# Optimization experiments

Measured on AMD Instinct MI355X. Metric: run time of the kernel, lower is better.

Reference implementation:

```python
import jax, jax.numpy as jnp
from jax import lax
import numpy as np

B, N, D_IN = 8, 8192, 16
GROUP_NUM, K = 512, 32
OUT_DIM, N_BLOCKS, DIM_EXP = 256, 2, 2
PREV_DIM = OUT_DIM // DIM_EXP   # 128
MID = OUT_DIM // 2              # bottleneck width in FeatureTransform
C_EXP = 2 * PREV_DIM + 3        # linear1 input channels
EPS = 1e-5                      # BatchNorm eps (eval mode, running stats mean=0 var=1)


def setup_inputs() -> dict:
    ks = jax.random.split(jax.random.key(0), 8)
    return {
        "xyz": jax.random.normal(ks[0], (B, N, 3), jnp.float32),
        "feat": jax.random.normal(ks[1], (B, N, D_IN), jnp.float32),
        "w_embed": jax.random.normal(ks[2], (PREV_DIM, D_IN), jnp.float32) * 0.1,
        "b_embed": jnp.zeros((PREV_DIM,), jnp.float32),
        "g_embed": jnp.ones((PREV_DIM,), jnp.float32),
        "be_embed": jnp.zeros((PREV_DIM,), jnp.float32),
        "w_lin1": jax.random.normal(ks[3], (OUT_DIM, C_EXP), jnp.float32) * 0.05,
        "g_lin1": jnp.ones((OUT_DIM,), jnp.float32),
        "be_lin1": jnp.zeros((OUT_DIM,), jnp.float32),
        "down_w": jax.random.normal(ks[4], (N_BLOCKS, MID, OUT_DIM), jnp.float32) * 0.05,
        "down_b": jnp.zeros((N_BLOCKS, MID), jnp.float32),
        "gd": jnp.ones((N_BLOCKS, MID), jnp.float32),
        "bd": jnp.zeros((N_BLOCKS, MID), jnp.float32),
        "up_w": jax.random.normal(ks[5], (N_BLOCKS, OUT_DIM, MID), jnp.float32) * 0.05,
        "up_b": jnp.zeros((N_BLOCKS, OUT_DIM), jnp.float32),
        "gu": jnp.ones((N_BLOCKS, OUT_DIM), jnp.float32),
        "bu": jnp.zeros((N_BLOCKS, OUT_DIM), jnp.float32),
    }


def _bn(x, g, b, axis):
    # eval-mode BatchNorm with running mean=0, var=1
    shp = [1] * x.ndim
    shp[axis] = -1
    return x / jnp.sqrt(1.0 + EPS) * g.reshape(shp) + b.reshape(shp)


def _fps(xyz, n):
    # deterministic FPS (eval mode): start from point farthest from origin
    Bb, Nn, _ = xyz.shape
    cur0 = jnp.argmax(jnp.sum(xyz * xyz, -1), axis=1)          # [B]
    mind0 = jnp.full((Bb, Nn), 1e10, xyz.dtype)

    def step(carry, _):
        cur, mind = carry
        c = jnp.take_along_axis(xyz, cur[:, None, None], axis=1)  # [B,1,3]
        mind = jnp.minimum(mind, jnp.sum((xyz - c) ** 2, -1))
        return (jnp.argmax(mind, axis=1), mind), cur

    _, sel = lax.scan(step, (cur0, mind0), None, length=n)     # sel: [n,B]
    return sel.T                                               # [B,n]


def _gather(points, idx):
    # points [B,N,C], idx [B,...] -> [B,...,C]
    Bb = points.shape[0]
    flat = idx.reshape(Bb, -1)
    out = jnp.take_along_axis(points, flat[:, :, None], axis=1)
    return out.reshape(idx.shape + (points.shape[-1],))


def _knn(k, ref, query):
    # squared dists, clamped at 0 as in pairwise_sq_dist
    d = (jnp.sum(query * query, -1)[:, :, None]
         + jnp.sum(ref * ref, -1)[:, None, :]
         - 2.0 * jnp.einsum('bsc,bnc->bsn', query, ref))
    d = jnp.maximum(d, 0.0)
    _, idx = lax.top_k(-d, k)
    return idx  # [B,S,k]


def reference(xyz, feat, w_embed, b_embed, g_embed, be_embed, w_lin1, g_lin1, be_lin1,
              down_w, down_b, gd, bd, up_w, up_b, gu, bu):
    # PointEmbed: conv1d(1x1) + BN + ReLU on per-point features -> [B,N,PREV_DIM]
    f0 = jnp.einsum('bnc,dc->bnd', feat, w_embed) + b_embed
    f0 = jax.nn.relu(_bn(f0, g_embed, be_embed, axis=2))

    # FpsKnnGroup
    sel = _fps(xyz, GROUP_NUM)                  # [B,G]
    lc_xyz = _gather(xyz, sel)                  # [B,G,3]
    lc_feat = _gather(f0, sel)                  # [B,G,PREV_DIM]
    nn_idx = _knn(K, xyz, lc_xyz)               # [B,G,K]
    knn_xyz = _gather(xyz, nn_idx)              # [B,G,K,3]
    knn_feat = jnp.concatenate([_gather(f0, nn_idx), knn_xyz], axis=-1)  # [B,G,K,PREV+3]

    # LocalGeoAgg, norm_type='mn40'
    anchor = lc_xyz[:, :, None, :]
    rel_raw = knn_xyz - anchor
    std = jnp.std(rel_raw, ddof=1) + 1e-5       # torch .std() is unbiased
    knn_xyz_n = rel_raw / std
    Bc = knn_feat.shape[0]
    expanded = jnp.concatenate(
        [knn_feat, jnp.broadcast_to(lc_feat[:, :, None, :], (Bc, GROUP_NUM, K, PREV_DIM))],
        axis=-1)                                # [B,G,K,C_EXP]
    x = jnp.einsum('bgkc,dc->bdgk', expanded, w_lin1)   # linear1 (no bias)
    x = jax.nn.relu(_bn(x, g_lin1, be_lin1, axis=1))    # [B,OUT_DIM,G,K]

    # GaussianPosEnc: rel = normalized knn_xyz (perm) minus raw lc_xyz center
    rel = knn_xyz_n.transpose(0, 3, 1, 2) - lc_xyz.transpose(0, 2, 1)[:, :, :, None]
    w = jnp.exp(-jnp.linalg.norm(rel, axis=1) / 2.0)    # sigma=1 -> 2*sigma^2=2
    x = x * w[:, None, :, :]

    # FeatureTransform residual bottlenecks
    for i in range(N_BLOCKS):
        h = jnp.einsum('bcgk,mc->bmgk', x, down_w[i]) + down_b[i][None, :, None, None]
        h = jax.nn.relu(_bn(h, gd[i], bd[i], axis=1))
        h = jnp.einsum('bcgk,mc->bmgk', h, up_w[i]) + up_b[i][None, :, None, None]
        h = _bn(h, gu[i], bu[i], axis=1)
        x = jax.nn.relu(h + x)

    # MaxMeanPool over K
    return jnp.max(x, axis=-1) + jnp.mean(x, axis=-1)   # [B,OUT_DIM,G]
```

## Files before the change

kernel.cpp:

```cpp
#include <hip/hip_runtime.h>

#define B_ 8
#define N_ 8192
#define DIN_ 16
#define G_ 512
#define K_ 32
#define OD_ 256
#define PD_ 128
#define MD_ 128
#define CE_ 259
#define EST 168
#define XST2 264
#define HST 136
#define AL1K 160

typedef __attribute__((ext_vector_type(8))) short short8t;
typedef __attribute__((ext_vector_type(4))) float f32x4;
#define MFMA16(a, b, c) __builtin_amdgcn_mfma_f32_16x16x32_bf16((a), (b), (c), 0, 0, 0)

__device__ __forceinline__ ushort bf16_rne(float x) {
    unsigned u = __float_as_uint(x);
    return (ushort)((u + 0x7FFFu + ((u >> 16) & 1u)) >> 16);
}
__device__ __forceinline__ void bf16_split(float x, ushort& h, ushort& l) {
    h = bf16_rne(x);
    float hf = __uint_as_float((unsigned)h << 16);
    l = bf16_rne(x - hf);
}

#define DPP_STEP_MAXF(x, ctrl) { int _t = __builtin_amdgcn_update_dpp(            \
        __float_as_int(x), __float_as_int(x), (ctrl), 0xF, 0xF, false);           \
        (x) = fmaxf((x), __int_as_float(_t)); }
#define DPP_STEP_MINF(x, ctrl) { int _t = __builtin_amdgcn_update_dpp(            \
        __float_as_int(x), __float_as_int(x), (ctrl), 0xF, 0xF, false);           \
        (x) = fminf((x), __int_as_float(_t)); }
#define DPP_STEP_MINU(x, ctrl) { int _t = __builtin_amdgcn_update_dpp(            \
        (int)(x), (int)(x), (ctrl), 0xF, 0xF, false);                             \
        unsigned _u = (unsigned)_t; (x) = ((x) < _u) ? (x) : _u; }

__device__ __forceinline__ float wave_max_f32(float x) {
    DPP_STEP_MAXF(x, 0x121); DPP_STEP_MAXF(x, 0x122);
    DPP_STEP_MAXF(x, 0x124); DPP_STEP_MAXF(x, 0x128);
    DPP_STEP_MAXF(x, 0x142); DPP_STEP_MAXF(x, 0x143);
    return __int_as_float(__builtin_amdgcn_readlane(__float_as_int(x), 63));
}
__device__ __forceinline__ float wave_min_f32(float x) {
    DPP_STEP_MINF(x, 0x121); DPP_STEP_MINF(x, 0x122);
    DPP_STEP_MINF(x, 0x124); DPP_STEP_MINF(x, 0x128);
    DPP_STEP_MINF(x, 0x142); DPP_STEP_MINF(x, 0x143);
    return __int_as_float(__builtin_amdgcn_readlane(__float_as_int(x), 63));
}
__device__ __forceinline__ unsigned wave_min_u32(unsigned x) {
    DPP_STEP_MINU(x, 0x121); DPP_STEP_MINU(x, 0x122);
    DPP_STEP_MINU(x, 0x124); DPP_STEP_MINU(x, 0x128);
    DPP_STEP_MINU(x, 0x142); DPP_STEP_MINU(x, 0x143);
    return (unsigned)__builtin_amdgcn_readlane((int)x, 63);
}

__global__ __launch_bounds__(256)
void prep_kernel(const float* __restrict__ w_lin1, const float* __restrict__ down_w,
                 const float* __restrict__ up_w, const float* __restrict__ w_embed,
                 float* __restrict__ wta, float* __restrict__ wEtg,
                 ushort* __restrict__ alf, ushort* __restrict__ adf,
                 ushort* __restrict__ auf) {
    int i = blockIdx.x * blockDim.x + threadIdx.x;
    if (i < PD_ * OD_) {
        int j = i >> 8, c = i & 255;
        wta[i] = w_lin1[c * CE_ + 131 + j];
    }
    if (i < DIN_ * PD_) {
        int r = i >> 7, c = i & 127;
        wEtg[i] = w_embed[c * DIN_ + r];
    }
    if (i < 5120) {
        int lane = i & 63, t = i >> 6;
        int kbi = t % 5, mtile = t / 5;
        int m = mtile * 16 + (lane & 15), g16 = lane >> 4;
        int dst = i * 8;
#pragma unroll
        for (int j = 0; j < 8; ++j) {
            int k = kbi * 32 + g16 * 8 + j;
            float v = (k < 131) ? w_lin1[m * CE_ + k] : 0.f;
            ushort h, l; bf16_split(v, h, l);
            alf[dst + j] = h; alf[dst + j + 40960] = l;
        }
    }
    if (i < 8192) {
        int lane = i & 63, t = i >> 6;
        int kbi = t & 7, mtile = (t >> 3) & 7, l = t >> 6;
        int m = mtile * 16 + (lane & 15), g16 = lane >> 4;
        int dst = i * 8;
#pragma unroll
        for (int j = 0; j < 8; ++j) {
            int k = kbi * 32 + g16 * 8 + j;
            float v = down_w[(l * MD_ + m) * OD_ + k];
            ushort h, lo; bf16_split(v, h, lo);
            adf[dst + j] = h; adf[dst + j + 65536] = lo;
        }
    }
    if (i < 8192) {
        int lane = i & 63, t = i >> 6;
        int kbi = t & 3, mtile = (t >> 2) & 15, l = t >> 6;
        int m = mtile * 16 + (lane & 15), g16 = lane >> 4;
        int dst = i * 8;
#pragma unroll
        for (int j = 0; j < 8; ++j) {
            int k = kbi * 32 + g16 * 8 + j;
            float v = up_w[(l * OD_ + m) * MD_ + k];
            ushort h, lo; bf16_split(v, h, lo);
            auf[dst + j] = h; auf[dst + j + 65536] = lo;
        }
    }
}

__global__ __launch_bounds__(512)
void fps_kernel(const float* __restrict__ xyz, int* __restrict__ sel) {
#pragma clang fp contract(off)
    __shared__ unsigned long long wred[2][8];
    __shared__ float4 wpt[2][8];
    __shared__ int sel_s[G_];
    int b = blockIdx.x, tid = threadIdx.x;
    const float* xb = xyz + (size_t)b * N_ * 3;
    float px[16], py[16], pz[16], mind[16];
    float bv = -1.f, bx = 0.f, by = 0.f, bz = 0.f; int bi = 0;
#pragma unroll
    for (int j = 0; j < 16; ++j) {
        int idx = tid + j * 512;
        px[j] = xb[idx * 3]; py[j] = xb[idx * 3 + 1]; pz[j] = xb[idx * 3 + 2];
        mind[j] = 1e10f;
        float ss = (px[j] * px[j] + py[j] * py[j]) + pz[j] * pz[j];
        if (ss > bv) { bv = ss; bi = idx; bx = px[j]; by = py[j]; bz = pz[j]; }
    }
    int wv = tid >> 6;
    {
        float wm = wave_max_f32(bv);
        unsigned mi = (bv == wm) ? (unsigned)bi : 0xFFFFFFFFu;
        unsigned wi = wave_min_u32(mi);
        if ((tid & 63) == 0)
            wred[0][wv] = ((unsigned long long)__float_as_uint(wm) << 32)
                        | (unsigned long long)(0xFFFFFFFFu - wi);
        if (bv == wm && (unsigned)bi == wi)
            wpt[0][wv] = make_float4(bx, by, bz, 0.f);
    }
    __syncthreads();
    unsigned long long best = wred[0][0]; int wb = 0;
#pragma unroll
    for (int i = 1; i < 8; ++i) { unsigned long long v = wred[0][i]; if (v > best) { best = v; wb = i; } }
    int cur = (int)(0xFFFFFFFFu - (unsigned)(best & 0xFFFFFFFFull));
    float4 cc = wpt[0][wb];
    float cx = cc.x, cy = cc.y, cz = cc.z;

    for (int it = 0; it < G_; ++it) {
        if (tid == 0) sel_s[it] = cur;
        bv = -1.f; bi = 0; bx = 0.f; by = 0.f; bz = 0.f;
#pragma unroll
        for (int j = 0; j < 16; ++j) {
            float dx = px[j] - cx, dy = py[j] - cy, dz = pz[j] - cz;
            float d = (dx * dx + dy * dy) + dz * dz;
            float m = fminf(mind[j], d); mind[j] = m;
            if (m > bv) { bv = m; bi = tid + j * 512; bx = px[j]; by = py[j]; bz = pz[j]; }
        }
        float wm = wave_max_f32(bv);
        unsigned mi = (bv == wm) ? (unsigned)bi : 0xFFFFFFFFu;
        unsigned wi = wave_min_u32(mi);
        int pb = (it + 1) & 1;
        if ((tid & 63) == 0)
            wred[pb][wv] = ((unsigned long long)__float_as_uint(wm) << 32)
                         | (unsigned long long)(0xFFFFFFFFu - wi);
        if (bv == wm && (unsigned)bi == wi)
            wpt[pb][wv] = make_float4(bx, by, bz, 0.f);
        __syncthreads();
        best = wred[pb][0]; wb = 0;
#pragma unroll
        for (int i = 1; i < 8; ++i) { unsigned long long v = wred[pb][i]; if (v > best) { best = v; wb = i; } }
        cur = (int)(0xFFFFFFFFu - (unsigned)(best & 0xFFFFFFFFull));
        cc = wpt[pb][wb];
        cx = cc.x; cy = cc.y; cz = cc.z;
    }
    __syncthreads();
    sel[b * G_ + tid] = sel_s[tid];
}

__global__ __launch_bounds__(256)
void knn_kernel(const float* __restrict__ xyz, const int* __restrict__ sel,
                int* __restrict__ nn) {
#pragma clang fp contract(off)
    __shared__ float dld[N_];
    __shared__ unsigned long long wred[2][4];
    __shared__ int nn_s[K_];
    int gb = blockIdx.x; int b = gb >> 9, s = gb & (G_ - 1);
    const float* xb = xyz + (size_t)b * N_ * 3;
    int q = sel[b * G_ + s];
    float qx = xb[q * 3], qy = xb[q * 3 + 1], qz = xb[q * 3 + 2];
    float qq = (qx * qx + qy * qy) + qz * qz;
    int tid = threadIdx.x;
    const float FINF = __builtin_inff();
    float lv = FINF; int li = tid;
#pragma unroll 4
    for (int j = 0; j < 32; ++j) {
        int n = tid + j * 256;
        float rx = xb[n * 3], ry = xb[n * 3 + 1], rz = xb[n * 3 + 2];
        float rr = (rx * rx + ry * ry) + rz * rz;
        float dt = (qx * rx + qy * ry) + qz * rz;
        float d = (qq + rr) - 2.0f * dt;
        d = fmaxf(d, 0.f);
        dld[n] = d;
        if (d < lv) { lv = d; li = n; }
    }
    {
        float wm = wave_min_f32(lv);
        unsigned mi = (lv == wm) ? (unsigned)li : 0xFFFFFFFFu;
        unsigned wi = wave_min_u32(mi);
        if ((tid & 63) == 0)
            wred[0][tid >> 6] = ((unsigned long long)__float_as_uint(wm) << 32)
                              | (unsigned long long)wi;
    }
    __syncthreads();
    unsigned long long best = wred[0][0];
#pragma unroll
    for (int i = 1; i < 4; ++i) { unsigned long long v = wred[0][i]; if (v < best) best = v; }
    int win = (int)(best & 0xFFFFFFFFull);

    for (int t = 0; t < K_; ++t) {
        if (tid == 0) nn_s[t] = win;
        if ((win & 255) == tid) {
            dld[win] = FINF;
            lv = FINF; li = tid;
            for (int j = 0; j < 32; ++j) {
                float d = dld[tid + j * 256];
                if (d < lv) { lv = d; li = tid + j * 256; }
            }
        }
        float wm = wave_min_f32(lv);
        unsigned mi = (lv == wm) ? (unsigned)li : 0xFFFFFFFFu;
        unsigned wi = wave_min_u32(mi);
        int pb = (t + 1) & 1;
        if ((tid & 63) == 0)
            wred[pb][tid >> 6] = ((unsigned long long)__float_as_uint(wm) << 32)
                               | (unsigned long long)wi;
        __syncthreads();
        best = wred[pb][0];
#pragma unroll
        for (int i = 1; i < 4; ++i) { unsigned long long v = wred[pb][i]; if (v < best) best = v; }
        win = (int)(best & 0xFFFFFFFFull);
    }
    if (tid < K_) nn[(size_t)gb * K_ + tid] = nn_s[tid];
}

__global__ void std_acc_kernel(const float* __restrict__ xyz, const int* __restrict__ sel,
                               const int* __restrict__ nn, double* __restrict__ acc) {
    int tot = B_ * G_ * K_;
    int stride = gridDim.x * blockDim.x;
    double ls = 0.0, lss = 0.0;
    for (int idx = blockIdx.x * blockDim.x + threadIdx.x; idx < tot; idx += stride) {
        int b = idx >> 14; int g = (idx >> 5) & (G_ - 1);
        int n = nn[idx]; int a = sel[b * G_ + g];
        const float* xb = xyz + (size_t)b * N_ * 3;
#pragma unroll
        for (int c = 0; c < 3; ++c) {
            float v = xb[n * 3 + c] - xb[a * 3 + c];
            ls += (double)v; lss += (double)v * (double)v;
        }
    }
#pragma unroll
    for (int off = 32; off > 0; off >>= 1) {
        ls += __shfl_down(ls, off); lss += __shfl_down(lss, off);
    }
    if ((threadIdx.x & 63) == 0) { atomicAdd(acc, ls); atomicAdd(acc + 1, lss); }
}

__global__ void std_fin_kernel(const double* __restrict__ acc, float* __restrict__ stdp) {
    double s = acc[0], ss = acc[1];
    double M = (double)(B_ * G_ * K_ * 3);
    double var = (ss - s * s / M) / (M - 1.0);
    stdp[0] = (float)sqrt(var) + 1e-5f;
}

__global__ __launch_bounds__(256, 3)
void group_kernel(const float* __restrict__ xyz, const float* __restrict__ feat,
                  const float* __restrict__ wEtg, const float* __restrict__ bE,
                  const float* __restrict__ gE, const float* __restrict__ beE,
                  const int* __restrict__ sel, const int* __restrict__ nn,
                  const float* __restrict__ wta,
                  const ushort* __restrict__ alf, const ushort* __restrict__ adf,
                  const ushort* __restrict__ auf,
                  const float* __restrict__ g_lin1, const float* __restrict__ be_lin1,
                  const float* __restrict__ down_b, const float* __restrict__ gd,
                  const float* __restrict__ bd,
                  const float* __restrict__ up_b, const float* __restrict__ gu,
                  const float* __restrict__ bu,
                  const float* __restrict__ stdp, float* __restrict__ out) {
    __shared__ __align__(16) ushort smem[25600];
    __shared__ float lcv_s[OD_];
    __shared__ float wk_s[K_];
    __shared__ int nns_s[K_];
    __shared__ float anch[3];
    ushort* XTh = smem;
    ushort* XTl = smem + 8448;
    ushort* HTh = smem + 16896;
    ushort* HTl = smem + 21248;
    ushort* Ehi = XTh;
    ushort* Elo = XTl;
    float* wEt = (float*)(smem + 16896);
    float* fL  = wEt + 2048;
    float* lcf = fL + 544;

    int gb = blockIdx.x; int b = gb >> 9, g = gb & (G_ - 1);
    int tid = threadIdx.x;
    const float* xb = xyz + (size_t)b * N_ * 3;
    int a = sel[b * G_ + g];
    if (tid < K_) nns_s[tid] = nn[(size_t)gb * K_ + tid];
    if (tid < 3)  anch[tid] = xb[a * 3 + tid];
    __syncthreads();

    for (int idx = tid; idx < DIN_ * PD_; idx += 256) wEt[idx] = wEtg[idx];
    const float* fb = feat + (size_t)b * N_ * DIN_;
    for (int idx = tid; idx < 33 * DIN_; idx += 256) {
        int k = idx >> 4, j = idx & 15;
        int n = (k < K_) ? nns_s[k] : a;
        fL[idx] = fb[(size_t)n * DIN_ + j];
    }
    __syncthreads();

    const float s_bn = 1.0f / sqrtf(1.0f + 1e-5f);
    for (int t = tid; t < 33 * 32; t += 256) {
        int k = t >> 5, c0 = (t & 31) * 4;
        const float* f = &fL[k * DIN_];
        float a0 = 0.f, a1 = 0.f, a2 = 0.f, a3 = 0.f;
#pragma unroll
        for (int i = 0; i < DIN_; ++i) {
            float4 w4 = *(const float4*)&wEt[i * PD_ + c0];
            float fv = f[i];
            a0 += w4.x * fv; a1 += w4.y * fv; a2 += w4.z * fv; a3 += w4.w * fv;
        }
        float4 b4  = *(const float4*)&bE[c0];
        float4 g4  = *(const float4*)&gE[c0];
        float4 be4 = *(const float4*)&beE[c0];
        float o0 = fmaxf((a0 + b4.x) * s_bn * g4.x + be4.x, 0.f);
        float o1 = fmaxf((a1 + b4.y) * s_bn * g4.y + be4.y, 0.f);
        float o2 = fmaxf((a2 + b4.z) * s_bn * g4.z + be4.z, 0.f);
        float o3 = fmaxf((a3 + b4.w) * s_bn * g4.w + be4.w, 0.f);
        if (k < K_) {
            ushort h0, l0, h1, l1, h2, l2, h3, l3;
            bf16_split(o0, h0, l0); bf16_split(o1, h1, l1);
            bf16_split(o2, h2, l2); bf16_split(o3, h3, l3);
            *(ushort4*)&Ehi[k * EST + c0] = make_ushort4(h0, h1, h2, h3);
            *(ushort4*)&Elo[k * EST + c0] = make_ushort4(l0, l1, l2, l3);
        } else {
            *(float4*)&lcf[c0] = make_float4(o0, o1, o2, o3);
        }
    }
    for (int idx = tid; idx < K_ * 32; idx += 256) {
        int k = idx >> 5, c = 128 + (idx & 31);
        ushort h = 0, l = 0;
        if (c < 131) { float v = xb[nns_s[k] * 3 + (c - 128)]; bf16_split(v, h, l); }
        Ehi[k * EST + c] = h; Elo[k * EST + c] = l;
    }
    if (tid < K_) {
#pragma clang fp contract(off)
        float sd = stdp[0];
        int n = nns_s[tid];
        float rx = (xb[n * 3]     - anch[0]) / sd - anch[0];
        float ry = (xb[n * 3 + 1] - anch[1]) / sd - anch[1];
        float rz = (xb[n * 3 + 2] - anch[2]) / sd - anch[2];
        float nrm = sqrtf((rx * rx + ry * ry) + rz * rz);
        wk_s[tid] = expf(-0.5f * nrm);
    }
    __syncthreads();
    {
        float s = 0.f;
        for (int j = 0; j < PD_; ++j) s += wta[j * OD_ + tid] * lcf[j];
        lcv_s[tid] = s;
    }
    __syncthreads();

    int wv = tid >> 6, lane = tid & 63;
    int g16 = lane >> 4, r16 = lane & 15;
    int lane8 = lane * 8;

    f32x4 accl[4][2];
#pragma unroll
    for (int mt = 0; mt < 4; ++mt) {
        int mc = 64 * wv + 16 * mt + 4 * g16;
        float4 lv = *(const float4*)&lcv_s[mc];
        f32x4 iv = {lv.x, lv.y, lv.z, lv.w};
        accl[mt][0] = iv; accl[mt][1] = iv;
    }
    {
        int eb0 = r16 * EST + g16 * 8;
        int eb1 = (r16 + 16) * EST + g16 * 8;
        for (int kbi = 0; kbi < 5; ++kbi) {
            int kb = kbi * 32;
            short8t eh0 = *(const short8t*)&Ehi[eb0 + kb];
            short8t el0 = *(const short8t*)&Elo[eb0 + kb];
            short8t eh1 = *(const short8t*)&Ehi[eb1 + kb];
            short8t el1 = *(const short8t*)&Elo[eb1 + kb];
#pragma unroll
            for (int mt = 0; mt < 4; ++mt) {
                const ushort* wp = alf + (((4 * wv + mt) * 5 + kbi) << 9) + lane8;
                short8t wh = *(const short8t*)wp;
                short8t wl = *(const short8t*)(wp + 40960);
                accl[mt][0] = MFMA16(wh, eh0, accl[mt][0]);
                accl[mt][1] = MFMA16(wh, eh1, accl[mt][1]);
                accl[mt][0] = MFMA16(wh, el0, accl[mt][0]);
                accl[mt][1] = MFMA16(wh, el1, accl[mt][1]);
                accl[mt][0] = MFMA16(wl, eh0, accl[mt][0]);
                accl[mt][1] = MFMA16(wl, eh1, accl[mt][1]);
            }
        }
    }
    __syncthreads();
    {
        float w0 = wk_s[r16], w1 = wk_s[r16 + 16];
#pragma unroll
        for (int mt = 0; mt < 4; ++mt) {
            int mc = 64 * wv + 16 * mt + 4 * g16;
            float4 gg = *(const float4*)&g_lin1[mc];
            float4 bb = *(const float4*)&be_lin1[mc];
            float ga[4] = {gg.x, gg.y, gg.z, gg.w};
            float ba[4] = {bb.x, bb.y, bb.z, bb.w};
            ushort h0[4], l0[4], h1[4], l1[4];
#pragma unroll
            for (int r = 0; r < 4; ++r) {
                float v0 = fmaxf(accl[mt][0][r] * s_bn * ga[r] + ba[r], 0.f) * w0;
                float v1 = fmaxf(accl[mt][1][r] * s_bn * ga[r] + ba[r], 0.f) * w1;
                bf16_split(v0, h0[r], l0[r]);
                bf16_split(v1, h1[r], l1[r]);
            }
            *(ushort4*)&XTh[r16 * XST2 + mc] = make_ushort4(h0[0], h0[1], h0[2], h0[3]);
            *(ushort4*)&XTl[r16 * XST2 + mc] = make_ushort4(l0[0], l0[1], l0[2], l0[3]);
            *(ushort4*)&XTh[(r16 + 16) * XST2 + mc] = make_ushort4(h1[0], h1[1], h1[2], h1[3]);
            *(ushort4*)&XTl[(r16 + 16) * XST2 + mc] = make_ushort4(l1[0], l1[1], l1[2], l1[3]);
        }
    }
    __syncthreads();

    int xbo0 = r16 * XST2 + g16 * 8;
    int xbo1 = (r16 + 16) * XST2 + g16 * 8;
    int hbo0 = r16 * HST + g16 * 8;
    int hbo1 = (r16 + 16) * HST + g16 * 8;
    const f32x4 zz = {0.f, 0.f, 0.f, 0.f};
    const float inv_k = 1.0f / 32.0f;

    for (int l = 0; l < 2; ++l) {
        f32x4 accd[2][2];
        accd[0][0] = zz; accd[0][1] = zz; accd[1][0] = zz; accd[1][1] = zz;
        for (int kbi = 0; kbi < 8; ++kbi) {
            int kb = kbi * 32;
            short8t xh0 = *(const short8t*)&XTh[xbo0 + kb];
            short8t xl0 = *(const short8t*)&XTl[xbo0 + kb];
            short8t xh1 = *(const short8t*)&XTh[xbo1 + kb];
            short8t xl1 = *(const short8t*)&XTl[xbo1 + kb];
#pragma unroll
            for (int mt = 0; mt < 2; ++mt) {
                const ushort* wp = adf + (((l * 8 + (2 * wv + mt)) * 8 + kbi) << 9) + lane8;
                short8t wh = *(const short8t*)wp;
                short8t wl = *(const short8t*)(wp + 65536);
                accd[mt][0] = MFMA16(wh, xh0, accd[mt][0]);
                accd[mt][1] = MFMA16(wh, xh1, accd[mt][1]);
                accd[mt][0] = MFMA16(wh, xl0, accd[mt][0]);
                accd[mt][1] = MFMA16(wh, xl1, accd[mt][1]);
                accd[mt][0] = MFMA16(wl, xh0, accd[mt][0]);
                accd[mt][1] = MFMA16(wl, xh1, accd[mt][1]);
            }
        }
#pragma unroll
        for (int mt = 0; mt < 2; ++mt) {
            int mc = 32 * wv + 16 * mt + 4 * g16;
            float4 db = *(const float4*)&down_b[l * MD_ + mc];
            float4 gv = *(const float4*)&gd[l * MD_ + mc];
            float4 bv = *(const float4*)&bd[l * MD_ + mc];
            float dba[4] = {db.x, db.y, db.z, db.w};
            float gva[4] = {gv.x, gv.y, gv.z, gv.w};
            float bva[4] = {bv.x, bv.y, bv.z, bv.w};
            ushort h0[4], l0[4], h1[4], l1[4];
#pragma unroll
            for (int r = 0; r < 4; ++r) {
                float v0 = fmaxf((accd[mt][0][r] + dba[r]) * s_bn * gva[r] + bva[r], 0.f);
                float v1 = fmaxf((accd[mt][1][r] + dba[r]) * s_bn * gva[r] + bva[r], 0.f);
                bf16_split(v0, h0[r], l0[r]);
                bf16_split(v1, h1[r], l1[r]);
            }
            *(ushort4*)&HTh[r16 * HST + mc] = make_ushort4(h0[0], h0[1], h0[2], h0[3]);
            *(ushort4*)&HTl[r16 * HST + mc] = make_ushort4(l0[0], l0[1], l0[2], l0[3]);
            *(ushort4*)&HTh[(r16 + 16) * HST + mc] = make_ushort4(h1[0], h1[1], h1[2], h1[3]);
            *(ushort4*)&HTl[(r16 + 16) * HST + mc] = make_ushort4(l1[0], l1[1], l1[2], l1[3]);
        }
        __syncthreads();

        f32x4 accu[4][2];
#pragma unroll
        for (int mt = 0; mt < 4; ++mt) { accu[mt][0] = zz; accu[mt][1] = zz; }
        for (int kbi = 0; kbi < 4; ++kbi) {
            int kb = kbi * 32;
            short8t hh0 = *(const short8t*)&HTh[hbo0 + kb];
            short8t hl0 = *(const short8t*)&HTl[hbo0 + kb];
            short8t hh1 = *(const short8t*)&HTh[hbo1 + kb];
            short8t hl1 = *(const short8t*)&HTl[hbo1 + kb];
#pragma unroll
            for (int mt = 0; mt < 4; ++mt) {
                const ushort* wp = auf + (((l * 16 + (4 * wv + mt)) * 4 + kbi) << 9) + lane8;
                short8t wh = *(const short8t*)wp;
                short8t wl = *(const short8t*)(wp + 65536);
                accu[mt][0] = MFMA16(wh, hh0, accu[mt][0]);
                accu[mt][1] = MFMA16(wh, hh1, accu[mt][1]);
                accu[mt][0] = MFMA16(wh, hl0, accu[mt][0]);
                accu[mt][1] = MFMA16(wh, hl1, accu[mt][1]);
                accu[mt][0] = MFMA16(wl, hh0, accu[mt][0]);
                accu[mt][1] = MFMA16(wl, hh1, accu[mt][1]);
            }
        }
#pragma unroll
        for (int mt = 0; mt < 4; ++mt) {
            int mc = 64 * wv + 16 * mt + 4 * g16;
            float4 ub = *(const float4*)&up_b[l * OD_ + mc];
            float4 gv = *(const float4*)&gu[l * OD_ + mc];
            float4 bv = *(const float4*)&bu[l * OD_ + mc];
            float uba[4] = {ub.x, ub.y, ub.z, ub.w};
            float gva[4] = {gv.x, gv.y, gv.z, gv.w};
            float bva[4] = {bv.x, bv.y, bv.z, bv.w};
            ushort4 xh0 = *(const ushort4*)&XTh[r16 * XST2 + mc];
            ushort4 xl0 = *(const ushort4*)&XTl[r16 * XST2 + mc];
            ushort4 xh1 = *(const ushort4*)&XTh[(r16 + 16) * XST2 + mc];
            ushort4 xl1 = *(const ushort4*)&XTl[(r16 + 16) * XST2 + mc];
            ushort xha0[4] = {xh0.x, xh0.y, xh0.z, xh0.w};
            ushort xla0[4] = {xl0.x, xl0.y, xl0.z, xl0.w};
            ushort xha1[4] = {xh1.x, xh1.y, xh1.z, xh1.w};
            ushort xla1[4] = {xl1.x, xl1.y, xl1.z, xl1.w};
            float nx0[4], nx1[4];
#pragma unroll
            for (int r = 0; r < 4; ++r) {
                float xf0 = __uint_as_float((unsigned)xha0[r] << 16) + __uint_as_float((unsigned)xla0[r] << 16);
                float xf1 = __uint_as_float((unsigned)xha1[r] << 16) + __uint_as_float((unsigned)xla1[r] << 16);
                float v0 = (accu[mt][0][r] + uba[r]) * s_bn * gva[r] + bva[r];
                float v1 = (accu[mt][1][r] + uba[r]) * s_bn * gva[r] + bva[r];
                nx0[r] = fmaxf(v0 + xf0, 0.f);
                nx1[r] = fmaxf(v1 + xf1, 0.f);
            }
            if (l == 0) {
                ushort h0[4], l0[4], h1[4], l1[4];
#pragma unroll
                for (int r = 0; r < 4; ++r) {
                    bf16_split(nx0[r], h0[r], l0[r]);
                    bf16_split(nx1[r], h1[r], l1[r]);
                }
                *(ushort4*)&XTh[r16 * XST2 + mc] = make_ushort4(h0[0], h0[1], h0[2], h0[3]);
                *(ushort4*)&XTl[r16 * XST2 + mc] = make_ushort4(l0[0], l0[1], l0[2], l0[3]);
                *(ushort4*)&XTh[(r16 + 16) * XST2 + mc] = make_ushort4(h1[0], h1[1], h1[2], h1[3]);
                *(ushort4*)&XTl[(r16 + 16) * XST2 + mc] = make_ushort4(l1[0], l1[1], l1[2], l1[3]);
            } else {
#pragma unroll
                for (int r = 0; r < 4; ++r) {
                    float mx = fmaxf(nx0[r], nx1[r]);
                    float sm = nx0[r] + nx1[r];
#pragma unroll
                    for (int off = 1; off < 16; off <<= 1) {
                        mx = fmaxf(mx, __shfl_xor(mx, off));
                        sm += __shfl_xor(sm, off);
                    }
                    if (r16 == 0)
                        out[((size_t)(b * OD_ + mc + r)) * G_ + g] = mx + sm * inv_k;
                }
            }
        }
        __syncthreads();
    }
}

extern "C" void kernel_launch(void* const* d_in, const int* in_sizes, int n_in,
                              void* d_out, int out_size, void* d_ws, size_t ws_size,
                              hipStream_t stream) {
    const float* xyz     = (const float*)d_in[0];
    const float* feat    = (const float*)d_in[1];
    const float* w_embed = (const float*)d_in[2];
    const float* b_embed = (const float*)d_in[3];
    const float* g_embed = (const float*)d_in[4];
    const float* be_embed= (const float*)d_in[5];
    const float* w_lin1  = (const float*)d_in[6];
    const float* g_lin1  = (const float*)d_in[7];
    const float* be_lin1 = (const float*)d_in[8];
    const float* down_w  = (const float*)d_in[9];
    const float* down_b  = (const float*)d_in[10];
    const float* gd      = (const float*)d_in[11];
    const float* bd      = (const float*)d_in[12];
    const float* up_w    = (const float*)d_in[13];
    const float* up_b    = (const float*)d_in[14];
    const float* gu      = (const float*)d_in[15];
    const float* bu      = (const float*)d_in[16];
    float* out = (float*)d_out;

    char* w = (char*)d_ws;
    float* wta   = (float*)w;  w += PD_ * OD_ * 4;
    float* wEtg  = (float*)w;  w += DIN_ * PD_ * 4;
    ushort* alf  = (ushort*)w; w += 2 * 40960 * 2;
    ushort* adf  = (ushort*)w; w += 2 * 65536 * 2;
    ushort* auf  = (ushort*)w; w += 2 * 65536 * 2;
    int* sel     = (int*)w;    w += B_ * G_ * 4;
    int* nn      = (int*)w;    w += B_ * G_ * K_ * 4;
    double* acc  = (double*)w; w += 16;
    float* stdp  = (float*)w;

    hipMemsetAsync(acc, 0, 2 * sizeof(double), stream);
    prep_kernel<<<256, 256, 0, stream>>>(w_lin1, down_w, up_w, w_embed,
                                         wta, wEtg, alf, adf, auf);
    fps_kernel<<<B_, 512, 0, stream>>>(xyz, sel);
    knn_kernel<<<B_ * G_, 256, 0, stream>>>(xyz, sel, nn);
    std_acc_kernel<<<256, 256, 0, stream>>>(xyz, sel, nn, acc);
    std_fin_kernel<<<1, 1, 0, stream>>>(acc, stdp);
    group_kernel<<<B_ * G_, 256, 0, stream>>>(xyz, feat, wEtg, b_embed, g_embed, be_embed,
        sel, nn, wta, alf, adf, auf, g_lin1, be_lin1, down_b, gd, bd, up_b, gu, bu, stdp, out);
}
```

Before: 1.102 ms.

## Stage FPS points in LDS, pack distance math into float2, drop winner-coordinate broadcast

The FPS kernel now copies the batch's xyz into shared memory as separate x/y/z arrays. Each thread keeps its 16 points as packed float2 vectors so the distance and min-update can use packed FP32 ops. Instead of the winning thread writing its coordinates to shared memory, every thread reads the new centroid from the shared copy by index. This simplifies the per-iteration argmax and cuts register moves in the serial 512-iteration loop, at the cost of 96KB of LDS and an extra shared read per iteration.

```diff
diff --git a/kernel.cpp b/kernel.cpp
--- a/kernel.cpp
+++ b/kernel.cpp
@@ -16,6 +16,7 @@
 
 typedef __attribute__((ext_vector_type(8))) short short8t;
 typedef __attribute__((ext_vector_type(4))) float f32x4;
+typedef __attribute__((ext_vector_type(2))) float v2f;
 #define MFMA16(a, b, c) __builtin_amdgcn_mfma_f32_16x16x32_bf16((a), (b), (c), 0, 0, 0)
 
 __device__ __forceinline__ ushort bf16_rne(float x) {
@@ -116,21 +117,30 @@
 __global__ __launch_bounds__(512)
 void fps_kernel(const float* __restrict__ xyz, int* __restrict__ sel) {
 #pragma clang fp contract(off)
+    __shared__ float sx[N_], sy[N_], sz[N_];
     __shared__ unsigned long long wred[2][8];
-    __shared__ float4 wpt[2][8];
     __shared__ int sel_s[G_];
     int b = blockIdx.x, tid = threadIdx.x;
     const float* xb = xyz + (size_t)b * N_ * 3;
-    float px[16], py[16], pz[16], mind[16];
-    float bv = -1.f, bx = 0.f, by = 0.f, bz = 0.f; int bi = 0;
-#pragma unroll
-    for (int j = 0; j < 16; ++j) {
-        int idx = tid + j * 512;
-        px[j] = xb[idx * 3]; py[j] = xb[idx * 3 + 1]; pz[j] = xb[idx * 3 + 2];
-        mind[j] = 1e10f;
-        float ss = (px[j] * px[j] + py[j] * py[j]) + pz[j] * pz[j];
-        if (ss > bv) { bv = ss; bi = idx; bx = px[j]; by = py[j]; bz = pz[j]; }
-    }
+    for (int i = tid; i < N_; i += 512) {
+        sx[i] = xb[i * 3]; sy[i] = xb[i * 3 + 1]; sz[i] = xb[i * 3 + 2];
+    }
+    __syncthreads();
+    v2f px2[8], py2[8], pz2[8], mind2[8];
+    float bv = -1.f; int bj = 0;
+#pragma unroll
+    for (int p = 0; p < 8; ++p) {
+        int i0 = tid + (2 * p) * 512, i1 = tid + (2 * p + 1) * 512;
+        px2[p] = (v2f){sx[i0], sx[i1]};
+        py2[p] = (v2f){sy[i0], sy[i1]};
+        pz2[p] = (v2f){sz[i0], sz[i1]};
+        mind2[p] = (v2f){1e10f, 1e10f};
+        v2f ss = px2[p] * px2[p] + py2[p] * py2[p];
+        ss = ss + pz2[p] * pz2[p];
+        if (ss[0] > bv) { bv = ss[0]; bj = 2 * p; }
+        if (ss[1] > bv) { bv = ss[1]; bj = 2 * p + 1; }
+    }
+    int bi = tid + bj * 512;
     int wv = tid >> 6;
     {
         float wm = wave_max_f32(bv);
@@ -139,27 +149,31 @@
         if ((tid & 63) == 0)
             wred[0][wv] = ((unsigned long long)__float_as_uint(wm) << 32)
                         | (unsigned long long)(0xFFFFFFFFu - wi);
-        if (bv == wm && (unsigned)bi == wi)
-            wpt[0][wv] = make_float4(bx, by, bz, 0.f);
-    }
-    __syncthreads();
-    unsigned long long best = wred[0][0]; int wb = 0;
-#pragma unroll
-    for (int i = 1; i < 8; ++i) { unsigned long long v = wred[0][i]; if (v > best) { best = v; wb = i; } }
+    }
+    __syncthreads();
+    unsigned long long best = wred[0][0];
+#pragma unroll
+    for (int i = 1; i < 8; ++i) { unsigned long long v = wred[0][i]; if (v > best) best = v; }
     int cur = (int)(0xFFFFFFFFu - (unsigned)(best & 0xFFFFFFFFull));
-    float4 cc = wpt[0][wb];
-    float cx = cc.x, cy = cc.y, cz = cc.z;
 
     for (int it = 0; it < G_; ++it) {
         if (tid == 0) sel_s[it] = cur;
-        bv = -1.f; bi = 0; bx = 0.f; by = 0.f; bz = 0.f;
+        float cx = sx[cur], cy = sy[cur], cz = sz[cur];
+        v2f cx2 = (v2f){cx, cx}, cy2 = (v2f){cy, cy}, cz2 = (v2f){cz, cz};
+#pragma unroll
+        for (int p = 0; p < 8; ++p) {
+            v2f dx = px2[p] - cx2, dy = py2[p] - cy2, dz = pz2[p] - cz2;
+            v2f d = dx * dx + dy * dy;
+            d = d + dz * dz;
+            mind2[p] = __builtin_elementwise_min(mind2[p], d);
+        }
+        bv = -1.f; bj = 0;
 #pragma unroll
         for (int j = 0; j < 16; ++j) {
-            float dx = px[j] - cx, dy = py[j] - cy, dz = pz[j] - cz;
-            float d = (dx * dx + dy * dy) + dz * dz;
-            float m = fminf(mind[j], d); mind[j] = m;
-            if (m > bv) { bv = m; bi = tid + j * 512; bx = px[j]; by = py[j]; bz = pz[j]; }
-        }
+            float m = mind2[j >> 1][j & 1];
+            if (m > bv) { bv = m; bj = j; }
+        }
+        bi = tid + bj * 512;
         float wm = wave_max_f32(bv);
         unsigned mi = (bv == wm) ? (unsigned)bi : 0xFFFFFFFFu;
         unsigned wi = wave_min_u32(mi);
@@ -167,15 +181,11 @@
         if ((tid & 63) == 0)
             wred[pb][wv] = ((unsigned long long)__float_as_uint(wm) << 32)
                          | (unsigned long long)(0xFFFFFFFFu - wi);
-        if (bv == wm && (unsigned)bi == wi)
-            wpt[pb][wv] = make_float4(bx, by, bz, 0.f);
         __syncthreads();
-        best = wred[pb][0]; wb = 0;
-#pragma unroll
-        for (int i = 1; i < 8; ++i) { unsigned long long v = wred[pb][i]; if (v > best) { best = v; wb = i; } }
+        best = wred[pb][0];
+#pragma unroll
+        for (int i = 1; i < 8; ++i) { unsigned long long v = wred[pb][i]; if (v > best) best = v; }
         cur = (int)(0xFFFFFFFFu - (unsigned)(best & 0xFFFFFFFFull));
-        cc = wpt[pb][wb];
-        cx = cc.x; cy = cc.y; cz = cc.z;
     }
     __syncthreads();
     sel[b * G_ + tid] = sel_s[tid];
```

Result: faster. 947.9 us (-14.0%).
